# Kernel tuning notes

Hardware: AMD Instinct MI355X
Metric: run time of the kernel (lower is better)

Reference implementation:

```python
import jax, jax.numpy as jnp
import numpy as np

N, E, F_IN, H, L, E_FEAT, G, OUT = 100000, 1600000, 8, 128, 4, 16, 256, 256


def setup_inputs() -> dict:
    key = jax.random.key(0)
    ks = jax.random.split(key, 12)
    inp = {
        "x": jax.random.normal(ks[0], (N, F_IN), jnp.float32),
        "edge_index": jax.random.randint(ks[1], (2, E), 0, N),
        "edge_attr": jax.random.uniform(ks[2], (E, E_FEAT), jnp.float32),
        "batch": jnp.sort(jax.random.randint(ks[3], (N,), 0, G)),
        "emb_W": jax.random.normal(ks[4], (F_IN, H), jnp.float32) / np.sqrt(F_IN),
        "emb_b": jnp.zeros((H,), jnp.float32),
        "edge_W": jax.random.normal(ks[5], (L, E_FEAT, H), jnp.float32) / np.sqrt(E_FEAT),
        "edge_b": jnp.zeros((L, H), jnp.float32),
        "nn_W": jax.random.normal(ks[6], (L, H, H), jnp.float32) / np.sqrt(H),
        "nn_b": jnp.zeros((L, H), jnp.float32),
        "bn_g": jnp.ones((L, H), jnp.float32),
        "bn_b": jnp.zeros((L, H), jnp.float32),
        "lin_W": jax.random.normal(ks[7], (H, OUT), jnp.float32) / np.sqrt(H),
        "lin_b": jnp.zeros((OUT,), jnp.float32),
    }
    return inp


def reference(x, edge_index, edge_attr, batch, emb_W, emb_b, edge_W, edge_b,
              nn_W, nn_b, bn_g, bn_b, lin_W, lin_b):
    eps_bn = 1e-5
    src, dst = edge_index[0], edge_index[1]
    h = x @ emb_W + emb_b  # node embedding [N,H]
    for l in range(L):
        e = edge_attr @ edge_W[l] + edge_b[l]          # [E,H] edge embedding
        msg = jax.nn.relu(h[src] + e)                   # gather + message
        agg = jax.ops.segment_sum(msg, dst, num_segments=N)  # scatter-add
        hc = (h + agg) @ nn_W[l] + nn_b[l]             # GINE nn (eps=0)
        mu = jnp.mean(hc, axis=0)
        var = jnp.mean((hc - mu) ** 2, axis=0)          # biased var (train BN)
        hc = (hc - mu) * jax.lax.rsqrt(var + eps_bn) * bn_g[l] + bn_b[l]
        hc = jax.nn.gelu(hc, approximate=False)
        h = h + hc                                      # 'res' residual
    out = h @ lin_W + lin_b                             # [N,OUT]
    rep = jax.ops.segment_sum(out, batch, num_segments=G)  # global_add_pool
    return rep
```

## Files before the change

kernel.cpp:

```cpp
#include <hip/hip_runtime.h>
#include <hip/hip_fp16.h>
#include <math.h>

#define GG 256

typedef __attribute__((ext_vector_type(8))) short short8;
typedef __attribute__((ext_vector_type(4))) float f32x4;

__device__ __forceinline__ unsigned short f2bf(float x) {
  union { float f; unsigned u; } v; v.f = x;
  unsigned r = v.u + 0x7fff + ((v.u >> 16) & 1);
  return (unsigned short)(r >> 16);
}

__device__ __forceinline__ unsigned pack_h2(float a, float b) {
  __half2 h = __floats2half2_rn(a, b);
  return *(unsigned*)&h;
}

__global__ __launch_bounds__(256) void k_emb(const float* __restrict__ x,
    const float* __restrict__ W, const float* __restrict__ b,
    float* __restrict__ h, unsigned short* __restrict__ hb, int N) {
  int idx = blockIdx.x * 256 + threadIdx.x;
  if (idx >= N * 32) return;
  int n = idx >> 5, q = idx & 31;
  const float* xr = x + (size_t)n * 8;
  float xs[8];
#pragma unroll
  for (int k = 0; k < 8; ++k) xs[k] = xr[k];
  float4 acc = ((const float4*)b)[q];
#pragma unroll
  for (int k = 0; k < 8; ++k) {
    float4 w = ((const float4*)(W + (size_t)k * 128))[q];
    acc.x += xs[k] * w.x; acc.y += xs[k] * w.y;
    acc.z += xs[k] * w.z; acc.w += xs[k] * w.w;
  }
  ((float4*)h)[idx] = acc;
  ushort4 hv4 = make_ushort4(f2bf(acc.x), f2bf(acc.y), f2bf(acc.z), f2bf(acc.w));
  *(ushort4*)(hb + (size_t)idx * 4) = hv4;
}

__global__ __launch_bounds__(256) void k_wconv(const float* __restrict__ eW,
    unsigned* __restrict__ eW16) {
  int i = blockIdx.x * 256 + threadIdx.x;
  if (i >= 4096) return;
  float2 wp = *(const float2*)(eW + (size_t)i * 2);
  eW16[i] = pack_h2(wp.x, wp.y);
}

__global__ __launch_bounds__(256) void k_nnconv(const float* __restrict__ W,
    unsigned short* __restrict__ WT) {
  int i = blockIdx.x * 256 + threadIdx.x;
  if (i >= 4 * 128 * 128) return;
  int n = i & 127, k = (i >> 7) & 127, l = i >> 14;
  WT[((size_t)(l * 128 + n)) * 128 + k] = f2bf(W[i]);
}

__global__ void k_hist(const int* __restrict__ dst, int* __restrict__ deg, int E) {
  int e = blockIdx.x * blockDim.x + threadIdx.x;
  if (e < E) atomicAdd(&deg[dst[e]], 1);
}

__global__ __launch_bounds__(256) void k_scan_reduce(const int* __restrict__ deg,
    int* __restrict__ bsum, int N) {
  __shared__ int sd[256];
  int i = blockIdx.x * 256 + threadIdx.x;
  sd[threadIdx.x] = (i < N) ? deg[i] : 0;
  __syncthreads();
  for (int s = 128; s > 0; s >>= 1) {
    if (threadIdx.x < s) sd[threadIdx.x] += sd[threadIdx.x + s];
    __syncthreads();
  }
  if (threadIdx.x == 0) bsum[blockIdx.x] = sd[0];
}

__global__ __launch_bounds__(512) void k_scan_mid(int* bsum, int nb) {
  __shared__ int sd[512];
  int t = threadIdx.x;
  int v = (t < nb) ? bsum[t] : 0;
  sd[t] = v; __syncthreads();
  for (int d = 1; d < 512; d <<= 1) {
    int xv = (t >= d) ? sd[t - d] : 0;
    __syncthreads();
    sd[t] += xv;
    __syncthreads();
  }
  if (t < nb) bsum[t] = sd[t] - v;
}

__global__ __launch_bounds__(256) void k_scan_final(const int* __restrict__ deg,
    const int* __restrict__ bsum, int* __restrict__ offs,
    int* __restrict__ cursor, int N) {
  __shared__ int sd[256];
  int t = threadIdx.x;
  int i = blockIdx.x * 256 + t;
  int v = (i < N) ? deg[i] : 0;
  sd[t] = v; __syncthreads();
  for (int d = 1; d < 256; d <<= 1) {
    int xv = (t >= d) ? sd[t - d] : 0;
    __syncthreads();
    sd[t] += xv;
    __syncthreads();
  }
  int off = bsum[blockIdx.x] + sd[t] - v;
  if (i < N) {
    offs[i] = off; cursor[i] = off;
    if (i == N - 1) offs[N] = off + v;
  }
}

__global__ void k_fill(const int* __restrict__ src, const int* __restrict__ dst,
    const float* __restrict__ attr, int* __restrict__ cursor,
    int* __restrict__ csrc, uint4* __restrict__ cattr16, int E) {
  int e = blockIdx.x * blockDim.x + threadIdx.x;
  if (e >= E) return;
  int d = dst[e];
  int pos = atomicAdd(&cursor[d], 1);
  csrc[pos] = src[e];
  const float4* a = (const float4*)(attr + (size_t)e * 16);
  float4 a0 = a[0], a1 = a[1], a2 = a[2], a3 = a[3];
  uint4 o0, o1;
  o0.x = pack_h2(a0.x, a0.y); o0.y = pack_h2(a0.z, a0.w);
  o0.z = pack_h2(a1.x, a1.y); o0.w = pack_h2(a1.z, a1.w);
  o1.x = pack_h2(a2.x, a2.y); o1.y = pack_h2(a2.z, a2.w);
  o1.z = pack_h2(a3.x, a3.y); o1.w = pack_h2(a3.z, a3.w);
  cattr16[(size_t)pos * 2] = o0;
  cattr16[(size_t)pos * 2 + 1] = o1;
}

__global__ void k_gstart(const int* __restrict__ batch, int* __restrict__ gstart,
                         int N, int Gn) {
  int i = blockIdx.x * blockDim.x + threadIdx.x;
  if (i >= N) return;
  int b = batch[i];
  if (i == 0) { for (int g = 0; g <= b; ++g) gstart[g] = 0; }
  else { int bp = batch[i - 1]; for (int g = bp + 1; g <= b; ++g) gstart[g] = i; }
  if (i == N - 1) { for (int g = b + 1; g <= Gn; ++g) gstart[g] = N; }
}

__global__ __launch_bounds__(256) void k_edge_agg(const float* __restrict__ h,
    const unsigned* __restrict__ hb32,
    const uint4* __restrict__ cattr16, const int* __restrict__ csrc,
    const int* __restrict__ offs, const unsigned* __restrict__ eW16,
    const float* __restrict__ eb, unsigned* __restrict__ hpa16,
    float* __restrict__ cstats, int N) {
  int t = threadIdx.x;
  if (blockIdx.x == 0) cstats[t] = 0.f;
  int n = blockIdx.x * 4 + (t >> 6);
  if (n >= N) return;
  int l = t & 63;
  __half2 w2[16];
#pragma unroll
  for (int k = 0; k < 16; ++k) {
    unsigned u = eW16[k * 64 + l];
    w2[k] = *(__half2*)&u;
  }
  float2 bias = *(const float2*)(eb + 2 * l);
  const unsigned* hb_l = hb32 + l;
  int jb = offs[n], je = offs[n + 1];
  jb = __builtin_amdgcn_readfirstlane(jb);
  je = __builtin_amdgcn_readfirstlane(je);

#define EDGE(JJ, ACC)                                                       \
  {                                                                         \
    int s = csrc[(JJ)];                                                     \
    uint4 p0 = cattr16[(size_t)(JJ) * 2];                                   \
    uint4 p1 = cattr16[(size_t)(JJ) * 2 + 1];                               \
    unsigned u = hb_l[(size_t)s * 64];                                      \
    __half2 ev = __floats2half2_rn(0.f, 0.f);                               \
    const unsigned pw[8] = {p0.x, p0.y, p0.z, p0.w, p1.x, p1.y, p1.z, p1.w};\
    _Pragma("unroll")                                                       \
    for (int k = 0; k < 8; ++k) {                                           \
      __half2 ap = *(__half2*)&pw[k];                                       \
      ev = __hfma2(__half2half2(__low2half(ap)), w2[2 * k], ev);            \
      ev = __hfma2(__half2half2(__high2half(ap)), w2[2 * k + 1], ev);       \
    }                                                                       \
    float e0 = __low2float(ev), e1 = __high2float(ev);                      \
    union { unsigned uu; float ff; } c0, c1;                                \
    c0.uu = u << 16; c1.uu = u & 0xffff0000u;                               \
    ACC.x += fmaxf(e0 + bias.x + c0.ff, 0.f);                               \
    ACC.y += fmaxf(e1 + bias.y + c1.ff, 0.f);                               \
  }

  float2 a0 = make_float2(0.f, 0.f), a1 = a0, a2 = a0, a3 = a0;
  float2 a4 = a0, a5 = a0, a6 = a0, a7 = a0;
  int j = jb;
  for (; j + 8 <= je; j += 8) {
    EDGE(j, a0) EDGE(j + 1, a1) EDGE(j + 2, a2) EDGE(j + 3, a3)
    EDGE(j + 4, a4) EDGE(j + 5, a5) EDGE(j + 6, a6) EDGE(j + 7, a7)
  }
  if (j + 4 <= je) {
    EDGE(j, a0) EDGE(j + 1, a1) EDGE(j + 2, a2) EDGE(j + 3, a3)
    j += 4;
  }
  for (; j < je; ++j) EDGE(j, a0)
#undef EDGE
  float2 hvv = *(const float2*)(h + (size_t)n * 128 + 2 * l);
  float rx = hvv.x + (((a0.x + a1.x) + (a2.x + a3.x)) + ((a4.x + a5.x) + (a6.x + a7.x)));
  float ry = hvv.y + (((a0.y + a1.y) + (a2.y + a3.y)) + ((a4.y + a5.y) + (a6.y + a7.y)));
  hpa16[(size_t)n * 64 + l] = ((unsigned)f2bf(ry) << 16) | (unsigned)f2bf(rx);
}

__global__ __launch_bounds__(256) void k_gemm_mfma(
    const unsigned short* __restrict__ A16, const unsigned short* __restrict__ WT16,
    const float* __restrict__ bias, float* __restrict__ hc,
    float* __restrict__ cstats, int N) {
  __shared__ short a_lds[128 * 136];
  __shared__ short w_lds[128 * 136];
  int t = threadIdx.x;
  int rowbase = blockIdx.x * 128;
  {
    int r = t >> 1;
    int off = (t & 1) * 64;
    const short* ga = (const short*)A16 + (size_t)(rowbase + r) * 128 + off;
    short* la = &a_lds[r * 136 + off];
    const short* gw = (const short*)WT16 + (size_t)r * 128 + off;
    short* lw = &w_lds[r * 136 + off];
    if (rowbase + r < N) {
#pragma unroll
      for (int jj = 0; jj < 8; ++jj)
        *(uint4*)(la + jj * 8) = *(const uint4*)(ga + jj * 8);
    } else {
#pragma unroll
      for (int jj = 0; jj < 8; ++jj)
        *(uint4*)(la + jj * 8) = make_uint4(0, 0, 0, 0);
    }
#pragma unroll
    for (int jj = 0; jj < 8; ++jj)
      *(uint4*)(lw + jj * 8) = *(const uint4*)(gw + jj * 8);
  }
  __syncthreads();
  int w = t >> 6;
  int lane = t & 63;
  int l15 = lane & 15, quad = lane >> 4;
  f32x4 acc[2][8];
#pragma unroll
  for (int rt = 0; rt < 2; ++rt)
#pragma unroll
    for (int nt = 0; nt < 8; ++nt)
      acc[rt][nt] = (f32x4){0.f, 0.f, 0.f, 0.f};
#pragma unroll
  for (int kc = 0; kc < 4; ++kc) {
    int k0 = kc * 32 + quad * 8;
    short8 af0 = *(const short8*)&a_lds[(w * 32 + l15) * 136 + k0];
    short8 af1 = *(const short8*)&a_lds[(w * 32 + 16 + l15) * 136 + k0];
#pragma unroll
    for (int nt = 0; nt < 8; ++nt) {
      short8 bf = *(const short8*)&w_lds[(nt * 16 + l15) * 136 + k0];
      acc[0][nt] = __builtin_amdgcn_mfma_f32_16x16x32_bf16(af0, bf, acc[0][nt], 0, 0, 0);
      acc[1][nt] = __builtin_amdgcn_mfma_f32_16x16x32_bf16(af1, bf, acc[1][nt], 0, 0, 0);
    }
  }
  float sA[8], sQ[8];
#pragma unroll
  for (int nt = 0; nt < 8; ++nt) { sA[nt] = 0.f; sQ[nt] = 0.f; }
#pragma unroll
  for (int nt = 0; nt < 8; ++nt) {
    int col = nt * 16 + l15;
    float bv = bias[col];
#pragma unroll
    for (int rt = 0; rt < 2; ++rt) {
      int rbase = rowbase + w * 32 + rt * 16 + quad * 4;
#pragma unroll
      for (int reg = 0; reg < 4; ++reg) {
        int row = rbase + reg;
        float v = acc[rt][nt][reg] + bv;
        if (row < N) {
          hc[(size_t)row * 128 + col] = v;
          sA[nt] += v; sQ[nt] += v * v;
        }
      }
    }
  }
#pragma unroll
  for (int nt = 0; nt < 8; ++nt) {
    sA[nt] += __shfl_xor(sA[nt], 16);
    sA[nt] += __shfl_xor(sA[nt], 32);
    sQ[nt] += __shfl_xor(sQ[nt], 16);
    sQ[nt] += __shfl_xor(sQ[nt], 32);
  }
  __syncthreads();
  float* sdA = (float*)a_lds;
  float* sdQ = (float*)w_lds;
  if (quad == 0) {
#pragma unroll
    for (int nt = 0; nt < 8; ++nt) {
      sdA[w * 128 + nt * 16 + l15] = sA[nt];
      sdQ[w * 128 + nt * 16 + l15] = sQ[nt];
    }
  }
  __syncthreads();
  if (t < 128) {
    float s = sdA[t] + sdA[128 + t] + sdA[256 + t] + sdA[384 + t];
    float s2 = sdQ[t] + sdQ[128 + t] + sdQ[256 + t] + sdQ[384 + t];
    atomicAdd(&cstats[t], s);
    atomicAdd(&cstats[128 + t], s2);
  }
}

__global__ __launch_bounds__(256) void k_bn(const float* __restrict__ hc,
    const float* __restrict__ cstats,
    const float* __restrict__ g, const float* __restrict__ bb,
    float* __restrict__ h, unsigned short* __restrict__ hb, int N) {
  int idx = blockIdx.x * 256 + threadIdx.x;
  if (idx >= N * 32) return;
  int q = idx & 31;
  float invN = 1.f / (float)N;
  float4 cs = ((const float4*)cstats)[q];
  float4 cq = ((const float4*)cstats)[q + 32];
  float4 gv = ((const float4*)g)[q];
  float4 bv = ((const float4*)bb)[q];
  float4 v = ((const float4*)hc)[idx];
  float4 hv = ((const float4*)h)[idx];
#define BN1(X)                                                      \
  { float mu = cs.X * invN;                                         \
    float var = cq.X * invN - mu * mu;                              \
    float xn = (v.X - mu) * rsqrtf(var + 1e-5f) * gv.X + bv.X;      \
    hv.X += 0.5f * xn * (1.f + erff(xn * 0.70710678118654752f)); }
  BN1(x) BN1(y) BN1(z) BN1(w)
#undef BN1
  ((float4*)h)[idx] = hv;
  if (hb) {
    ushort4 hv4 = make_ushort4(f2bf(hv.x), f2bf(hv.y), f2bf(hv.z), f2bf(hv.w));
    *(ushort4*)(hb + (size_t)idx * 4) = hv4;
  }
}

__global__ __launch_bounds__(256) void k_poolfinal(const float* __restrict__ h,
    const int* __restrict__ gstart, const float* __restrict__ W,
    const float* __restrict__ b, float* __restrict__ out) {
  int g = blockIdx.x;
  int t = threadIdx.x, c = t & 127, half = t >> 7;
  int n0 = gstart[g], n1 = gstart[g + 1];
  float s = 0.f;
  for (int n = n0 + half; n < n1; n += 2) s += h[(size_t)n * 128 + c];
  __shared__ float ls[256];
  __shared__ float pr[128];
  ls[t] = s; __syncthreads();
  if (t < 128) pr[t] = ls[t] + ls[t + 128];
  __syncthreads();
  float cnt = (float)(n1 - n0);
  float acc = cnt * b[t];
#pragma unroll 8
  for (int k = 0; k < 128; ++k) acc += pr[k] * W[(size_t)k * 256 + t];
  out[(size_t)g * 256 + t] = acc;
}

extern "C" void kernel_launch(void* const* d_in, const int* in_sizes, int n_in,
                              void* d_out, int out_size, void* d_ws, size_t ws_size,
                              hipStream_t stream) {
  const float* x     = (const float*)d_in[0];
  const int*   eidx  = (const int*)d_in[1];
  const float* eattr = (const float*)d_in[2];
  const int*   batch = (const int*)d_in[3];
  const float* embW  = (const float*)d_in[4];
  const float* embB  = (const float*)d_in[5];
  const float* edgeW = (const float*)d_in[6];
  const float* edgeB = (const float*)d_in[7];
  const float* nnW   = (const float*)d_in[8];
  const float* nnB   = (const float*)d_in[9];
  const float* bnG   = (const float*)d_in[10];
  const float* bnB   = (const float*)d_in[11];
  const float* linW  = (const float*)d_in[12];
  const float* linB  = (const float*)d_in[13];
  float* out = (float*)d_out;

  int N = in_sizes[0] / 8;
  int E = in_sizes[1] / 2;
  const int* src = eidx;
  const int* dst = eidx + E;

  char* wptr = (char*)d_ws;
  auto alloc = [&](size_t bytes) {
    char* p = wptr; wptr += (bytes + 255) & ~(size_t)255; return p;
  };
  float* h      = (float*)alloc((size_t)N * 128 * 4);
  float* hc     = (float*)alloc((size_t)N * 128 * 4);
  unsigned short* hb = (unsigned short*)alloc((size_t)N * 128 * 2);
  unsigned* hpa16 = (unsigned*)alloc((size_t)N * 64 * 4);
  uint4* cattr16 = (uint4*)alloc((size_t)E * 32);
  int*   csrc   = (int*)alloc((size_t)E * 4);
  int*   offs   = (int*)alloc((size_t)(N + 1) * 4);
  int*   cursor = (int*)alloc((size_t)N * 4);
  int*   deg    = (int*)alloc((size_t)N * 4);
  int nb = (N + 255) / 256;
  int*   bsum   = (int*)alloc((size_t)nb * 4);
  float* cstats = (float*)alloc(256 * 4);
  unsigned* eW16 = (unsigned*)alloc(4096 * 4);
  unsigned short* WT16 = (unsigned short*)alloc(4 * 128 * 128 * 2);
  int*   gstart = (int*)alloc((size_t)(GG + 1) * 4);

  int q32 = (N * 32 + 255) / 256;

  hipMemsetAsync(deg, 0, (size_t)N * 4, stream);
  k_emb<<<q32, 256, 0, stream>>>(x, embW, embB, h, hb, N);
  k_wconv<<<16, 256, 0, stream>>>(edgeW, eW16);
  k_nnconv<<<256, 256, 0, stream>>>(nnW, WT16);
  k_hist<<<(E + 255) / 256, 256, 0, stream>>>(dst, deg, E);
  k_scan_reduce<<<nb, 256, 0, stream>>>(deg, bsum, N);
  k_scan_mid<<<1, 512, 0, stream>>>(bsum, nb);
  k_scan_final<<<nb, 256, 0, stream>>>(deg, bsum, offs, cursor, N);
  k_fill<<<(E + 255) / 256, 256, 0, stream>>>(src, dst, eattr, cursor, csrc, cattr16, E);
  k_gstart<<<(N + 255) / 256, 256, 0, stream>>>(batch, gstart, N, GG);

  int gblk = (N + 127) / 128;
  for (int l = 0; l < 4; ++l) {
    k_edge_agg<<<(N + 3) / 4, 256, 0, stream>>>(h, (const unsigned*)hb, cattr16, csrc,
        offs, eW16 + (size_t)l * 1024, edgeB + (size_t)l * 128, hpa16, cstats, N);
    k_gemm_mfma<<<gblk, 256, 0, stream>>>((const unsigned short*)hpa16,
        WT16 + (size_t)l * 128 * 128, nnB + (size_t)l * 128, hc, cstats, N);
    k_bn<<<q32, 256, 0, stream>>>(hc, cstats,
        bnG + (size_t)l * 128, bnB + (size_t)l * 128, h, (l == 3) ? nullptr : hb, N);
  }
  k_poolfinal<<<GG, 256, 0, stream>>>(h, gstart, linW, linB, out);
}
```

Measured before the change: 1.207 ms.

## Prefetch edge source indices in aggregation; load GEMM A fragments directly from global

The edge aggregation loop now batches eight edges at a time. It issues all eight gathered node-feature loads together and prefetches the next group's source indices, so the dependent index-then-gather load latency overlaps across iterations. Separately, the MFMA GEMM drops the LDS staging of the A tile. Each lane loads its bf16 A fragments straight from global memory into registers, which halves shared memory use and may raise occupancy. The costs are more live registers and uncoalesced 16-byte A loads, and the stats scratch now reuses the weight LDS buffer after a sync.

Result: slower. 1.269 ms (+5.2%).

```diff
diff --git a/kernel.cpp b/kernel.cpp
--- a/kernel.cpp
+++ b/kernel.cpp
@@ -161,14 +161,10 @@
   jb = __builtin_amdgcn_readfirstlane(jb);
   je = __builtin_amdgcn_readfirstlane(je);
 
-#define EDGE(JJ, ACC)                                                       \
+#define MLPADD(P0, P1, U, ACC)                                              \
   {                                                                         \
-    int s = csrc[(JJ)];                                                     \
-    uint4 p0 = cattr16[(size_t)(JJ) * 2];                                   \
-    uint4 p1 = cattr16[(size_t)(JJ) * 2 + 1];                               \
-    unsigned u = hb_l[(size_t)s * 64];                                      \
     __half2 ev = __floats2half2_rn(0.f, 0.f);                               \
-    const unsigned pw[8] = {p0.x, p0.y, p0.z, p0.w, p1.x, p1.y, p1.z, p1.w};\
+    const unsigned pw[8] = {P0.x, P0.y, P0.z, P0.w, P1.x, P1.y, P1.z, P1.w};\
     _Pragma("unroll")                                                       \
     for (int k = 0; k < 8; ++k) {                                           \
       __half2 ap = *(__half2*)&pw[k];                                       \
@@ -177,27 +173,54 @@
     }                                                                       \
     float e0 = __low2float(ev), e1 = __high2float(ev);                      \
     union { unsigned uu; float ff; } c0, c1;                                \
-    c0.uu = u << 16; c1.uu = u & 0xffff0000u;                               \
+    c0.uu = (U) << 16; c1.uu = (U) & 0xffff0000u;                           \
     ACC.x += fmaxf(e0 + bias.x + c0.ff, 0.f);                               \
     ACC.y += fmaxf(e1 + bias.y + c1.ff, 0.f);                               \
   }
 
-  float2 a0 = make_float2(0.f, 0.f), a1 = a0, a2 = a0, a3 = a0;
-  float2 a4 = a0, a5 = a0, a6 = a0, a7 = a0;
+  float2 acc[8];
+#pragma unroll
+  for (int i = 0; i < 8; ++i) acc[i] = make_float2(0.f, 0.f);
+
   int j = jb;
-  for (; j + 8 <= je; j += 8) {
-    EDGE(j, a0) EDGE(j + 1, a1) EDGE(j + 2, a2) EDGE(j + 3, a3)
-    EDGE(j + 4, a4) EDGE(j + 5, a5) EDGE(j + 6, a6) EDGE(j + 7, a7)
-  }
-  if (j + 4 <= je) {
-    EDGE(j, a0) EDGE(j + 1, a1) EDGE(j + 2, a2) EDGE(j + 3, a3)
-    j += 4;
-  }
-  for (; j < je; ++j) EDGE(j, a0)
-#undef EDGE
+  if (j + 8 <= je) {
+    int s_cur[8];
+#pragma unroll
+    for (int i = 0; i < 8; ++i) s_cur[i] = csrc[j + i];
+    for (; j + 8 <= je; j += 8) {
+      unsigned u[8];
+#pragma unroll
+      for (int i = 0; i < 8; ++i) u[i] = hb_l[(size_t)s_cur[i] * 64];
+      int s_nxt[8];
+#pragma unroll
+      for (int i = 0; i < 8; ++i) {
+        int jn = j + 8 + i;
+        if (jn > je - 1) jn = je - 1;
+        s_nxt[i] = csrc[jn];
+      }
+#pragma unroll
+      for (int i = 0; i < 8; ++i) {
+        uint4 p0 = cattr16[(size_t)(j + i) * 2];
+        uint4 p1 = cattr16[(size_t)(j + i) * 2 + 1];
+        MLPADD(p0, p1, u[i], acc[i])
+      }
+#pragma unroll
+      for (int i = 0; i < 8; ++i) s_cur[i] = s_nxt[i];
+    }
+  }
+  for (; j < je; ++j) {
+    int s = csrc[j];
+    uint4 p0 = cattr16[(size_t)j * 2];
+    uint4 p1 = cattr16[(size_t)j * 2 + 1];
+    unsigned u = hb_l[(size_t)s * 64];
+    MLPADD(p0, p1, u, acc[0])
+  }
+#undef MLPADD
   float2 hvv = *(const float2*)(h + (size_t)n * 128 + 2 * l);
-  float rx = hvv.x + (((a0.x + a1.x) + (a2.x + a3.x)) + ((a4.x + a5.x) + (a6.x + a7.x)));
-  float ry = hvv.y + (((a0.y + a1.y) + (a2.y + a3.y)) + ((a4.y + a5.y) + (a6.y + a7.y)));
+  float rx = hvv.x + (((acc[0].x + acc[1].x) + (acc[2].x + acc[3].x)) +
+                      ((acc[4].x + acc[5].x) + (acc[6].x + acc[7].x)));
+  float ry = hvv.y + (((acc[0].y + acc[1].y) + (acc[2].y + acc[3].y)) +
+                      ((acc[4].y + acc[5].y) + (acc[6].y + acc[7].y)));
   hpa16[(size_t)n * 64 + l] = ((unsigned)f2bf(ry) << 16) | (unsigned)f2bf(rx);
 }
 
@@ -205,34 +228,34 @@
     const unsigned short* __restrict__ A16, const unsigned short* __restrict__ WT16,
     const float* __restrict__ bias, float* __restrict__ hc,
     float* __restrict__ cstats, int N) {
-  __shared__ short a_lds[128 * 136];
   __shared__ short w_lds[128 * 136];
   int t = threadIdx.x;
   int rowbase = blockIdx.x * 128;
   {
     int r = t >> 1;
     int off = (t & 1) * 64;
-    const short* ga = (const short*)A16 + (size_t)(rowbase + r) * 128 + off;
-    short* la = &a_lds[r * 136 + off];
     const short* gw = (const short*)WT16 + (size_t)r * 128 + off;
     short* lw = &w_lds[r * 136 + off];
-    if (rowbase + r < N) {
-#pragma unroll
-      for (int jj = 0; jj < 8; ++jj)
-        *(uint4*)(la + jj * 8) = *(const uint4*)(ga + jj * 8);
-    } else {
-#pragma unroll
-      for (int jj = 0; jj < 8; ++jj)
-        *(uint4*)(la + jj * 8) = make_uint4(0, 0, 0, 0);
-    }
 #pragma unroll
     for (int jj = 0; jj < 8; ++jj)
       *(uint4*)(lw + jj * 8) = *(const uint4*)(gw + jj * 8);
   }
-  __syncthreads();
   int w = t >> 6;
   int lane = t & 63;
   int l15 = lane & 15, quad = lane >> 4;
+  short8 af[2][4];
+#pragma unroll
+  for (int rt = 0; rt < 2; ++rt) {
+    int row = rowbase + w * 32 + rt * 16 + l15;
+    bool ok = row < N;
+#pragma unroll
+    for (int kc = 0; kc < 4; ++kc) {
+      short8 v = (short8){0, 0, 0, 0, 0, 0, 0, 0};
+      if (ok) v = *(const short8*)((const short*)A16 + (size_t)row * 128 + kc * 32 + quad * 8);
+      af[rt][kc] = v;
+    }
+  }
+  __syncthreads();
   f32x4 acc[2][8];
 #pragma unroll
   for (int rt = 0; rt < 2; ++rt)
@@ -242,13 +265,11 @@
 #pragma unroll
   for (int kc = 0; kc < 4; ++kc) {
     int k0 = kc * 32 + quad * 8;
-    short8 af0 = *(const short8*)&a_lds[(w * 32 + l15) * 136 + k0];
-    short8 af1 = *(const short8*)&a_lds[(w * 32 + 16 + l15) * 136 + k0];
 #pragma unroll
     for (int nt = 0; nt < 8; ++nt) {
       short8 bf = *(const short8*)&w_lds[(nt * 16 + l15) * 136 + k0];
-      acc[0][nt] = __builtin_amdgcn_mfma_f32_16x16x32_bf16(af0, bf, acc[0][nt], 0, 0, 0);
-      acc[1][nt] = __builtin_amdgcn_mfma_f32_16x16x32_bf16(af1, bf, acc[1][nt], 0, 0, 0);
+      acc[0][nt] = __builtin_amdgcn_mfma_f32_16x16x32_bf16(af[0][kc], bf, acc[0][nt], 0, 0, 0);
+      acc[1][nt] = __builtin_amdgcn_mfma_f32_16x16x32_bf16(af[1][kc], bf, acc[1][nt], 0, 0, 0);
     }
   }
   float sA[8], sQ[8];
@@ -280,8 +301,8 @@
     sQ[nt] += __shfl_xor(sQ[nt], 32);
   }
   __syncthreads();
-  float* sdA = (float*)a_lds;
-  float* sdQ = (float*)w_lds;
+  float* sdA = (float*)w_lds;
+  float* sdQ = (float*)w_lds + 512;
   if (quad == 0) {
 #pragma unroll
     for (int nt = 0; nt < 8; ++nt) {
```
